# Kernel tuning notes

Hardware: AMD Instinct MI355X
Metric: run time of the kernel (lower is better)

Reference implementation:

```python
import jax, jax.numpy as jnp
import numpy as np
from jax.scipy.special import logsumexp

N, T, K, V = 32, 4096, 128, 50000

def setup_inputs() -> dict:
    key = jax.random.key(0)
    ks = jax.random.split(key, 6)
    return {
        "x": jax.random.randint(ks[0], (N, T), 0, V, dtype=jnp.int64),
        "start_w": jax.random.normal(ks[1], (K, 1), dtype=jnp.float32),
        "start_b": jax.random.normal(ks[2], (K,), dtype=jnp.float32),
        "cluster_trans_w": jax.random.uniform(ks[3], (K * K, 1), dtype=jnp.float32, minval=-1.0, maxval=1.0),
        "emb_cluster_w": jax.random.normal(ks[4], (K, K), dtype=jnp.float32),
        "cluster_vocab_w": jax.random.uniform(ks[5], (V, K), dtype=jnp.float32, minval=-1.0, maxval=1.0),
    }

def reference(x, start_w, start_b, cluster_trans_w, emb_cluster_w, cluster_vocab_w):
    # dummy = ones(N,1) => Linear(1,.) collapses to weight[:,0] (+ bias), identical per batch row
    tran = jax.nn.log_softmax(cluster_trans_w[:, 0].reshape(K, K), axis=-1)      # (K,K) log p(k'|k)
    alpha0 = jnp.broadcast_to(start_w[:, 0] + start_b, (N, K))                    # (N,K)
    # Emissions[k,v] = log_softmax_v(emb_cluster.weight[k] @ cluster_vocab.weight.T)
    emis_t = jax.nn.log_softmax(emb_cluster_w @ cluster_vocab_w.T, axis=-1).T     # (V,K)

    def step(alpha, w_t):
        a = logsumexp(alpha[:, :, None] + tran[None, :, :], axis=1)               # (N,K)
        a = a + emis_t[w_t]                                                        # gather emission log-probs
        return a, None

    alpha_T, _ = jax.lax.scan(step, alpha0, x.T)                                  # scan over T timesteps
    return -jnp.mean(logsumexp(alpha_T, axis=1))
```

## Files before the change

kernel.cpp:

```cpp
#include <hip/hip_runtime.h>

typedef unsigned int uint;
typedef unsigned short ushort;
typedef uint4 uint4_a __attribute__((may_alias));
typedef uint ui4v __attribute__((ext_vector_type(4)));
typedef float fx4 __attribute__((ext_vector_type(4)));
typedef short s8v __attribute__((ext_vector_type(8)));

__device__ __forceinline__ uint bfpack(float a, float b) {
  uint ua = __float_as_uint(a), ub = __float_as_uint(b);
  ua += 0x7fffu + ((ua >> 16) & 1u);
  ub += 0x7fffu + ((ub >> 16) & 1u);
  return (ua >> 16) | (ub & 0xffff0000u);
}
__device__ __forceinline__ float bflo(uint d) { return __uint_as_float(d << 16); }
__device__ __forceinline__ float bfhi(uint d) { return __uint_as_float(d & 0xffff0000u); }
__device__ __forceinline__ ushort bfr(float s) {
  return (ushort)((__float_as_uint(s) + 0x8000u) >> 16);
}

#if __has_builtin(__builtin_amdgcn_fdot2_f32_bf16)
#define HAVE_BFDOT 1
typedef __bf16 v2bf __attribute__((ext_vector_type(2)));
__device__ __forceinline__ float dot2bf(uint a, uint b, float c) {
  return __builtin_amdgcn_fdot2_f32_bf16(__builtin_bit_cast(v2bf, a),
                                         __builtin_bit_cast(v2bf, b), c, false);
}
#else
#define HAVE_BFDOT 0
#endif

__global__ void k_tran(const float* __restrict__ w, uint* __restrict__ Tcol) {
  __shared__ float rowLSE[128];
  int tid = threadIdx.x;
  const float4* w4 = (const float4*)(w + tid * 128);
  float se = 0.f;
  #pragma unroll 8
  for (int i = 0; i < 32; ++i) {
    float4 v = w4[i];
    se += __expf(v.x) + __expf(v.y) + __expf(v.z) + __expf(v.w);
  }
  rowLSE[tid] = __logf(se);
  __syncthreads();
  int c = tid;
  for (int j = 0; j < 64; ++j) {
    float a = __expf(w[(2 * j) * 128 + c]     - rowLSE[2 * j]);
    float b = __expf(w[(2 * j + 1) * 128 + c] - rowLSE[2 * j + 1]);
    Tcol[c * 64 + j] = bfpack(a, b);
  }
}

__global__ __launch_bounds__(256) void k_logits(const float* __restrict__ emb,
    const float* __restrict__ vocab, uint* __restrict__ qtbl,
    float* __restrict__ S_glob, int V) {
  __shared__ float S_part[128];
  int tid = threadIdx.x;
  int kt = tid & 15, vt = tid >> 4;
  int k0 = kt * 8;
  int vbase = blockIdx.x * 64 + vt * 4;
  if (tid < 128) S_part[tid] = 0.f;
  __syncthreads();

  float acc[4][8];
  #pragma unroll
  for (int i = 0; i < 4; ++i)
    #pragma unroll
    for (int r = 0; r < 8; ++r) acc[i][r] = 0.f;

  int vidx[4];
  #pragma unroll
  for (int i = 0; i < 4; ++i) { int vv = vbase + i; vidx[i] = (vv < V) ? vv : (V - 1); }

  const float4* emb4 = (const float4*)emb;
  const float4* voc4 = (const float4*)vocab;
  for (int jb = 0; jb < 32; ++jb) {
    float4 e4[8];
    #pragma unroll
    for (int r = 0; r < 8; ++r) e4[r] = emb4[(k0 + r) * 32 + jb];
    #pragma unroll
    for (int i = 0; i < 4; ++i) {
      float4 va = voc4[(size_t)vidx[i] * 32 + jb];
      #pragma unroll
      for (int r = 0; r < 8; ++r)
        acc[i][r] += va.x * e4[r].x + va.y * e4[r].y + va.z * e4[r].z + va.w * e4[r].w;
    }
  }

  float sume[8];
  #pragma unroll
  for (int r = 0; r < 8; ++r) sume[r] = 0.f;
  #pragma unroll
  for (int i = 0; i < 4; ++i) {
    int vv = vbase + i;
    if (vv < V) {
      #pragma unroll
      for (int r = 0; r < 8; ++r) sume[r] += __expf(acc[i][r]);
      uint4 st;
      st.x = bfpack(acc[i][0], acc[i][1]);
      st.y = bfpack(acc[i][2], acc[i][3]);
      st.z = bfpack(acc[i][4], acc[i][5]);
      st.w = bfpack(acc[i][6], acc[i][7]);
      *((uint4*)(qtbl + (size_t)vv * 64) + kt) = st;
    }
  }
  #pragma unroll
  for (int r = 0; r < 8; ++r) atomicAdd(&S_part[k0 + r], sume[r]);
  __syncthreads();
  if (tid < 128) atomicAdd(&S_glob[tid], S_part[tid]);
}

__global__ __launch_bounds__(256) void k_qtab(uint* __restrict__ qtbl,
    const float* __restrict__ S_glob, float* __restrict__ Emax, int V) {
  int tid = threadIdx.x;
  int l = tid & 63;
  int v = blockIdx.x * 4 + (tid >> 6);
  if (v >= V) return;
  float2 S2 = ((const float2*)S_glob)[l];
  float z0 = __logf(S2.x), z1 = __logf(S2.y);
  size_t off = (size_t)v * 64 + l;
  uint d = qtbl[off];
  float e0 = bflo(d) - z0, e1 = bfhi(d) - z1;
  float m = fmaxf(e0, e1);
  #pragma unroll
  for (int s = 1; s < 64; s <<= 1) m = fmaxf(m, __shfl_xor(m, s, 64));
  float q0 = __expf(e0 - m), q1 = __expf(e1 - m);
  qtbl[off] = bfpack(q0, q1);
  if (l == 0) Emax[v] = m;
}

#define REPB(M) M(0,0) M(0,1) M(0,2) M(0,3) M(1,0) M(1,1) M(1,2) M(1,3) \
                M(2,0) M(2,1) M(2,2) M(2,3) M(3,0) M(3,1) M(3,2) M(3,3) \
                M(4,0) M(4,1) M(4,2) M(4,3) M(5,0) M(5,1) M(5,2) M(5,3) \
                M(6,0) M(6,1) M(6,2) M(6,3) M(7,0) M(7,1) M(7,2) M(7,3)

#define MFMA(a, b, c) __builtin_amdgcn_mfma_f32_16x16x32_bf16( \
    __builtin_bit_cast(s8v, a), __builtin_bit_cast(s8v, b), c, 0, 0, 0)

#define NTCHAIN(nt, BIN) \
  fx4 cc##nt = MFMA(tb##nt##_0, BIN##0, zz4); \
  cc##nt = MFMA(tb##nt##_1, BIN##1, cc##nt); \
  cc##nt = MFMA(tb##nt##_2, BIN##2, cc##nt); \
  cc##nt = MFMA(tb##nt##_3, BIN##3, cc##nt);

#define PKPAIR(CCA, CCB, QA, QB, DOUT) { \
  float f0 = bflo(QA.x) * rs, f1 = bfhi(QA.x) * rs; \
  float f2 = bflo(QA.y) * rs, f3 = bfhi(QA.y) * rs; \
  float s0 = CCA.x * f0, s1 = CCA.y * f1, s2 = CCA.z * f2, s3 = CCA.w * f3; \
  fm = fmaxf(fm, fmaxf(fmaxf(s0, s1), fmaxf(s2, s3))); \
  uint p0, p1, p2, p3; \
  asm("v_cvt_pk_bf16_f32 %0, %1, %2" : "=v"(p0) : "v"(s0), "v"(s1)); \
  asm("v_cvt_pk_bf16_f32 %0, %1, %2" : "=v"(p1) : "v"(s2), "v"(s3)); \
  float g0 = bflo(QB.x) * rs, g1 = bfhi(QB.x) * rs; \
  float g2 = bflo(QB.y) * rs, g3 = bfhi(QB.y) * rs; \
  float t0 = CCB.x * g0, t1 = CCB.y * g1, t2 = CCB.z * g2, t3 = CCB.w * g3; \
  fm = fmaxf(fm, fmaxf(fmaxf(t0, t1), fmaxf(t2, t3))); \
  asm("v_cvt_pk_bf16_f32 %0, %1, %2" : "=v"(p2) : "v"(t0), "v"(t1)); \
  asm("v_cvt_pk_bf16_f32 %0, %1, %2" : "=v"(p3) : "v"(t2), "v"(t3)); \
  DOUT.x = p0; DOUT.y = p1; DOUT.z = p2; DOUT.w = p3; }

#define PKPAIR_NR(CCA, CCB, QA, QB, DOUT) { \
  float s0 = CCA.x * bflo(QA.x), s1 = CCA.y * bfhi(QA.x); \
  float s2 = CCA.z * bflo(QA.y), s3 = CCA.w * bfhi(QA.y); \
  uint p0, p1, p2, p3; \
  asm("v_cvt_pk_bf16_f32 %0, %1, %2" : "=v"(p0) : "v"(s0), "v"(s1)); \
  asm("v_cvt_pk_bf16_f32 %0, %1, %2" : "=v"(p1) : "v"(s2), "v"(s3)); \
  float t0 = CCB.x * bflo(QB.x), t1 = CCB.y * bfhi(QB.x); \
  float t2 = CCB.z * bflo(QB.y), t3 = CCB.w * bfhi(QB.y); \
  asm("v_cvt_pk_bf16_f32 %0, %1, %2" : "=v"(p2) : "v"(t0), "v"(t1)); \
  asm("v_cvt_pk_bf16_f32 %0, %1, %2" : "=v"(p3) : "v"(t2), "v"(t3)); \
  DOUT.x = p0; DOUT.y = p1; DOUT.z = p2; DOUT.w = p3; }

#define QLD(dst, tk, i) dst = *(const uint2*)(qtbl + ((size_t)(tk) << 6) + 8 * (i) + 2 * quad);

#define QRELOAD(Q, TKREG, FBASE) \
  QLD(Q##0, TKREG, 0) QLD(Q##1, TKREG, 1) QLD(Q##2, TKREG, 2) QLD(Q##3, TKREG, 3) \
  QLD(Q##4, TKREG, 4) QLD(Q##5, TKREG, 5) QLD(Q##6, TKREG, 6) QLD(Q##7, TKREG, 7) \
  { int fi_ = (FBASE) + 4; if (fi_ > 511) fi_ = 511; TKREG = xseg[fi_]; }

#define FOLD_RS(BIN, BOUT, Q, TKREG, FBASE) { \
  rs = 1.0f / fmA;  llacc += __log2f(fmA); \
  NTCHAIN(0, BIN) NTCHAIN(1, BIN) NTCHAIN(2, BIN) NTCHAIN(3, BIN) \
  NTCHAIN(4, BIN) NTCHAIN(5, BIN) NTCHAIN(6, BIN) NTCHAIN(7, BIN) \
  float fm = 0.f; \
  PKPAIR(cc0, cc1, Q##0, Q##1, BOUT##0) \
  PKPAIR(cc2, cc3, Q##2, Q##3, BOUT##1) \
  PKPAIR(cc4, cc5, Q##4, Q##5, BOUT##2) \
  PKPAIR(cc6, cc7, Q##6, Q##7, BOUT##3) \
  QRELOAD(Q, TKREG, FBASE) \
  fm = fmaxf(fm, __shfl_xor(fm, 16, 64)); \
  fm = fmaxf(fm, __shfl_xor(fm, 32, 64)); \
  fmA = fmaxf(fm, 1e-33f); \
}

#define FOLD_NR(BIN, BOUT, Q, TKREG, FBASE) { \
  NTCHAIN(0, BIN) NTCHAIN(1, BIN) NTCHAIN(2, BIN) NTCHAIN(3, BIN) \
  NTCHAIN(4, BIN) NTCHAIN(5, BIN) NTCHAIN(6, BIN) NTCHAIN(7, BIN) \
  PKPAIR_NR(cc0, cc1, Q##0, Q##1, BOUT##0) \
  PKPAIR_NR(cc2, cc3, Q##2, Q##3, BOUT##1) \
  PKPAIR_NR(cc4, cc5, Q##4, Q##5, BOUT##2) \
  PKPAIR_NR(cc6, cc7, Q##6, Q##7, BOUT##3) \
  QRELOAD(Q, TKREG, FBASE) \
}

__global__ __attribute__((amdgpu_flat_work_group_size(512, 512), amdgpu_waves_per_eu(2)))
void k_seg(const int* __restrict__ x, const uint* __restrict__ Tcol,
           const uint* __restrict__ qtbl, uint* __restrict__ Pst,
           float* __restrict__ LLseg) {
  int tid = threadIdx.x;
  int wv = tid >> 6, l = tid & 63, c = l & 15, quad = l >> 4;
  int blk = blockIdx.x;
  const int* xseg = x + (size_t)(blk >> 3) * 4096 + (size_t)(blk & 7) * 512;

  #define DECLB(nt, ks) ui4v tb##nt##_##ks;
  REPB(DECLB)
  {
    #define LOADB(nt, ks) { \
      const uint2* t2_ = (const uint2*)(Tcol + (size_t)(16 * (nt) + c) * 64 + 16 * (ks) + 2 * quad); \
      uint2 lo_ = t2_[0], hi_ = t2_[4]; \
      tb##nt##_##ks.x = lo_.x; tb##nt##_##ks.y = lo_.y; \
      tb##nt##_##ks.z = hi_.x; tb##nt##_##ks.w = hi_.y; }
    REPB(LOADB)
    #define PINB(nt, ks) asm volatile("" : "+a"(tb##nt##_##ks));
    REPB(PINB)
  }

  ui4v Ba0, Ba1, Ba2, Ba3, Bb0, Bb1, Bb2, Bb3;
  {
    uint iv = (quad == (c >> 2)) ? (0x3F80u << (16 * (c & 1))) : 0u;
    int dsel = ((c >> 1) & 1) + 2 * (wv & 1);
    int kssel = wv >> 1;
    Ba0.x = (kssel == 0 && dsel == 0) ? iv : 0u;
    Ba0.y = (kssel == 0 && dsel == 1) ? iv : 0u;
    Ba0.z = (kssel == 0 && dsel == 2) ? iv : 0u;
    Ba0.w = (kssel == 0 && dsel == 3) ? iv : 0u;
    Ba1.x = (kssel == 1 && dsel == 0) ? iv : 0u;
    Ba1.y = (kssel == 1 && dsel == 1) ? iv : 0u;
    Ba1.z = (kssel == 1 && dsel == 2) ? iv : 0u;
    Ba1.w = (kssel == 1 && dsel == 3) ? iv : 0u;
    Ba2.x = (kssel == 2 && dsel == 0) ? iv : 0u;
    Ba2.y = (kssel == 2 && dsel == 1) ? iv : 0u;
    Ba2.z = (kssel == 2 && dsel == 2) ? iv : 0u;
    Ba2.w = (kssel == 2 && dsel == 3) ? iv : 0u;
    Ba3.x = (kssel == 3 && dsel == 0) ? iv : 0u;
    Ba3.y = (kssel == 3 && dsel == 1) ? iv : 0u;
    Ba3.z = (kssel == 3 && dsel == 2) ? iv : 0u;
    Ba3.w = (kssel == 3 && dsel == 3) ? iv : 0u;
    Bb0.x = 0u; Bb0.y = 0u; Bb0.z = 0u; Bb0.w = 0u;
    Bb1 = Bb0; Bb2 = Bb0; Bb3 = Bb0;
  }

  float rs = 1.0f, llacc = 0.0f, fmA = 1.0f;
  fx4 zz4; zz4.x = 0.f; zz4.y = 0.f; zz4.z = 0.f; zz4.w = 0.f;

  int tk0 = xseg[0], tk1 = xseg[1];
  int tkA = xseg[2], tkB = xseg[3];
  uint2 qc0, qc1, qc2, qc3, qc4, qc5, qc6, qc7;
  uint2 qn0, qn1, qn2, qn3, qn4, qn5, qn6, qn7;
  QLD(qc0, tk0, 0) QLD(qc1, tk0, 1) QLD(qc2, tk0, 2) QLD(qc3, tk0, 3)
  QLD(qc4, tk0, 4) QLD(qc5, tk0, 5) QLD(qc6, tk0, 6) QLD(qc7, tk0, 7)
  QLD(qn0, tk1, 0) QLD(qn1, tk1, 1) QLD(qn2, tk1, 2) QLD(qn3, tk1, 3)
  QLD(qn4, tk1, 4) QLD(qn5, tk1, 5) QLD(qn6, tk1, 6) QLD(qn7, tk1, 7)

  if (wv & 1) __builtin_amdgcn_s_sleep(8);

  for (int f4 = 0; f4 < 128; ++f4) {
    int f = f4 * 4;
    FOLD_RS(Ba, Bb, qc, tkA, f)
    FOLD_NR(Bb, Ba, qn, tkB, f + 1)
    FOLD_NR(Ba, Bb, qc, tkA, f + 2)
    FOLD_NR(Bb, Ba, qn, tkB, f + 3)
  }

  size_t pb = (size_t)blk * 8192 + (size_t)(16 * wv + c) * 64;
  uint2 st;
  st.x = Ba0.x; st.y = Ba0.y; *(uint2*)(Pst + pb +  0 + 2 * quad) = st;
  st.x = Ba0.z; st.y = Ba0.w; *(uint2*)(Pst + pb +  8 + 2 * quad) = st;
  st.x = Ba1.x; st.y = Ba1.y; *(uint2*)(Pst + pb + 16 + 2 * quad) = st;
  st.x = Ba1.z; st.y = Ba1.w; *(uint2*)(Pst + pb + 24 + 2 * quad) = st;
  st.x = Ba2.x; st.y = Ba2.y; *(uint2*)(Pst + pb + 32 + 2 * quad) = st;
  st.x = Ba2.z; st.y = Ba2.w; *(uint2*)(Pst + pb + 40 + 2 * quad) = st;
  st.x = Ba3.x; st.y = Ba3.y; *(uint2*)(Pst + pb + 48 + 2 * quad) = st;
  st.x = Ba3.z; st.y = Ba3.w; *(uint2*)(Pst + pb + 56 + 2 * quad) = st;
  if (quad == 0)
    LLseg[(size_t)blk * 128 + 16 * wv + c] = llacc * 0.6931471805599453f;
}

__global__ __launch_bounds__(64, 1) void k_comb(
    const float* __restrict__ start_w, const float* __restrict__ start_b,
    const uint* __restrict__ Pst, const float* __restrict__ LLseg,
    float* __restrict__ chainLL) {
  __shared__ uint al[64] __attribute__((aligned(16)));
  int n = blockIdx.x, l = threadIdx.x;
  float a0i = start_w[2 * l] + start_b[2 * l];
  float a1i = start_w[2 * l + 1] + start_b[2 * l + 1];
  float m = fmaxf(a0i, a1i);
  #pragma unroll
  for (int s = 1; s < 64; s <<= 1) m = fmaxf(m, __shfl_xor(m, s, 64));
  float p0 = __expf(a0i - m), p1 = __expf(a1i - m);
  float tot = p0 + p1;
  #pragma unroll
  for (int s = 1; s < 64; s <<= 1) tot += __shfl_xor(tot, s, 64);
  float LLacc = m + __logf(tot);
  float inv = 1.0f / tot;
  p0 *= inv; p1 *= inv;
  const uint4_a* u4 = (const uint4_a*)al;

  for (int s = 0; s < 8; ++s) {
    float La = LLseg[(size_t)(n * 8 + s) * 128 + 2 * l];
    float Lb = LLseg[(size_t)(n * 8 + s) * 128 + 2 * l + 1];
    float g = fmaxf(La, Lb);
    #pragma unroll
    for (int sh = 1; sh < 64; sh <<= 1) g = fmaxf(g, __shfl_xor(g, sh, 64));
    al[l] = bfpack(p0 * __expf(La - g), p1 * __expf(Lb - g));

    const uint* pb = Pst + (size_t)(n * 8 + s) * 8192;
    float o0 = 0.f, o1 = 0.f;
    #pragma unroll
    for (int i = 0; i < 16; ++i) {
      uint4 uu = u4[i];
      #pragma unroll
      for (int d = 0; d < 4; ++d) {
        uint ad = (d == 0) ? uu.x : (d == 1) ? uu.y : (d == 2) ? uu.z : uu.w;
        uint P0 = pb[(8 * i + 2 * d) * 64 + l];
        uint P1 = pb[(8 * i + 2 * d + 1) * 64 + l];
        float alo = bflo(ad), ahi = bfhi(ad);
        o0 = fmaf(alo, bflo(P0), o0); o0 = fmaf(ahi, bflo(P1), o0);
        o1 = fmaf(alo, bfhi(P0), o1); o1 = fmaf(ahi, bfhi(P1), o1);
      }
    }
    float tt = o0 + o1;
    #pragma unroll
    for (int sh = 1; sh < 64; sh <<= 1) tt += __shfl_xor(tt, sh, 64);
    LLacc += g + __logf(tt);
    float it = 1.0f / tt;
    p0 = o0 * it; p1 = o1 * it;
  }
  if (l == 0) chainLL[n] = LLacc;
}

#define RLU(i) ((uint)__builtin_amdgcn_readlane((int)ud, rbase + (i)))
#if HAVE_BFDOT
#define DOTS \
  uint u0=RLU(0),u1=RLU(1),u2=RLU(2),u3=RLU(3),u4=RLU(4),u5=RLU(5),u6=RLU(6),u7=RLU(7), \
       u8=RLU(8),u9=RLU(9),u10=RLU(10),u11=RLU(11),u12=RLU(12),u13=RLU(13),u14=RLU(14),u15=RLU(15); \
  float A0 = dot2bf(u0, tA0.x, 0.f), A1 = dot2bf(u1, tA0.y, 0.f); \
  float A2 = dot2bf(u2, tA0.z, 0.f), A3 = dot2bf(u3, tA0.w, 0.f); \
  float B0 = dot2bf(u0, tB0.x, 0.f), B1 = dot2bf(u1, tB0.y, 0.f); \
  float B2 = dot2bf(u2, tB0.z, 0.f), B3 = dot2bf(u3, tB0.w, 0.f); \
  A0 = dot2bf(u4, tA1.x, A0); A1 = dot2bf(u5, tA1.y, A1); \
  A2 = dot2bf(u6, tA1.z, A2); A3 = dot2bf(u7, tA1.w, A3); \
  B0 = dot2bf(u4, tB1.x, B0); B1 = dot2bf(u5, tB1.y, B1); \
  B2 = dot2bf(u6, tB1.z, B2); B3 = dot2bf(u7, tB1.w, B3); \
  A0 = dot2bf(u8, tA2.x, A0); A1 = dot2bf(u9, tA2.y, A1); \
  A2 = dot2bf(u10, tA2.z, A2); A3 = dot2bf(u11, tA2.w, A3); \
  B0 = dot2bf(u8, tB2.x, B0); B1 = dot2bf(u9, tB2.y, B1); \
  B2 = dot2bf(u10, tB2.z, B2); B3 = dot2bf(u11, tB2.w, B3); \
  A0 = dot2bf(u12, tA3.x, A0); A1 = dot2bf(u13, tA3.y, A1); \
  A2 = dot2bf(u14, tA3.z, A2); A3 = dot2bf(u15, tA3.w, A3); \
  B0 = dot2bf(u12, tB3.x, B0); B1 = dot2bf(u13, tB3.y, B1); \
  B2 = dot2bf(u14, tB3.z, B2); B3 = dot2bf(u15, tB3.w, B3); \
  float Asum = (A0 + A1) + (A2 + A3), Bsum = (B0 + B1) + (B2 + B3);
#else
#define ACC2(i, AA, BB) { uint tu = RLU(i); float lo = bflo(tu), hi = bfhi(tu); \
  AA += lo * fa##i.x; AA += hi * fa##i.y; BB += lo * fb##i.x; BB += hi * fb##i.y; }
#define DOTS \
  float A0 = 0.f, A1 = 0.f, A2 = 0.f, A3 = 0.f; \
  float B0 = 0.f, B1 = 0.f, B2 = 0.f, B3 = 0.f; \
  ACC2(0, A0, B0) ACC2(1, A1, B1) ACC2(2, A2, B2) ACC2(3, A3, B3) \
  ACC2(4, A0, B0) ACC2(5, A1, B1) ACC2(6, A2, B2) ACC2(7, A3, B3) \
  ACC2(8, A0, B0) ACC2(9, A1, B1) ACC2(10, A2, B2) ACC2(11, A3, B3) \
  ACC2(12, A0, B0) ACC2(13, A1, B1) ACC2(14, A2, B2) ACC2(15, A3, B3) \
  float Asum = (A0 + A1) + (A2 + A3), Bsum = (B0 + B1) + (B2 + B3);
#endif

#define STEPF(j, p) { \
  DOTS \
  *(float2*)&partLDS[(p) * 640 + l * 10 + 2 * wv] = make_float2(Asum, Bsum); \
  asm volatile("s_waitcnt lgkmcnt(0)\ns_barrier" ::: "memory"); \
  const float2* pr = (const float2*)&partLDS[(p) * 640 + l * 10]; \
  float2 x0 = pr[0], x1 = pr[1], x2 = pr[2], x3 = pr[3]; \
  float s0 = (x0.x + x1.x) + (x2.x + x3.x); \
  float s1 = (x0.y + x1.y) + (x2.y + x3.y); \
  float nu0 = s0 * bflo(qc##j), nu1 = s1 * bfhi(qc##j); \
  qc##j = qtbl[(size_t)tk##j * 64 + l]; \
  tk##j = xrow[(tbase + (j) + 16) & 4095]; \
  if ((j) == 7) { \
    float tt = nu0 + nu1; \
    for (int s = 1; s < 64; s <<= 1) tt += __shfl_xor(tt, s, 64); \
    LLacc += __logf(tt); \
    float it = 1.0f / tt; nu0 *= it; nu1 *= it; \
  } \
  ud = bfpack(nu0, nu1); }

__global__ __launch_bounds__(256, 1) void k_chain(const int* __restrict__ x,
    const float* __restrict__ start_w, const float* __restrict__ start_b,
    const uint* __restrict__ Tcol, const uint* __restrict__ qtbl,
    float* __restrict__ chainLL) {
  __shared__ float partLDS[1280];
  int n = blockIdx.x;
  int l = threadIdx.x & 63;
  int wv = __builtin_amdgcn_readfirstlane((int)(threadIdx.x >> 6));
  int rbase = wv * 16;
  const int* xrow = x + (size_t)n * 4096;

  const uint4* ca = (const uint4*)(Tcol + (2 * l) * 64 + rbase);
  const uint4* cb = (const uint4*)(Tcol + (2 * l + 1) * 64 + rbase);
  uint4 tA0 = ca[0], tA1 = ca[1], tA2 = ca[2], tA3 = ca[3];
  uint4 tB0 = cb[0], tB1 = cb[1], tB2 = cb[2], tB3 = cb[3];
#if !HAVE_BFDOT
  float2 fa0 = make_float2(bflo(tA0.x), bfhi(tA0.x)), fa1 = make_float2(bflo(tA0.y), bfhi(tA0.y));
  float2 fa2 = make_float2(bflo(tA0.z), bfhi(tA0.z)), fa3 = make_float2(bflo(tA0.w), bfhi(tA0.w));
  float2 fa4 = make_float2(bflo(tA1.x), bfhi(tA1.x)), fa5 = make_float2(bflo(tA1.y), bfhi(tA1.y));
  float2 fa6 = make_float2(bflo(tA1.z), bfhi(tA1.z)), fa7 = make_float2(bflo(tA1.w), bfhi(tA1.w));
  float2 fa8 = make_float2(bflo(tA2.x), bfhi(tA2.x)), fa9 = make_float2(bflo(tA2.y), bfhi(tA2.y));
  float2 fa10 = make_float2(bflo(tA2.z), bfhi(tA2.z)), fa11 = make_float2(bflo(tA2.w), bfhi(tA2.w));
  float2 fa12 = make_float2(bflo(tA3.x), bfhi(tA3.x)), fa13 = make_float2(bflo(tA3.y), bfhi(tA3.y));
  float2 fa14 = make_float2(bflo(tA3.z), bfhi(tA3.z)), fa15 = make_float2(bflo(tA3.w), bfhi(tA3.w));
  float2 fb0 = make_float2(bflo(tB0.x), bfhi(tB0.x)), fb1 = make_float2(bflo(tB0.y), bfhi(tB0.y));
  float2 fb2 = make_float2(bflo(tB0.z), bfhi(tB0.z)), fb3 = make_float2(bflo(tB0.w), bfhi(tB0.w));
  float2 fb4 = make_float2(bflo(tB1.x), bfhi(tB1.x)), fb5 = make_float2(bflo(tB1.y), bfhi(tB1.y));
  float2 fb6 = make_float2(bflo(tB1.z), bfhi(tB1.z)), fb7 = make_float2(bflo(tB1.w), bfhi(tB1.w));
  float2 fb8 = make_float2(bflo(tB2.x), bfhi(tB2.x)), fb9 = make_float2(bflo(tB2.y), bfhi(tB2.y));
  float2 fb10 = make_float2(bflo(tB2.z), bfhi(tB2.z)), fb11 = make_float2(bflo(tB2.w), bfhi(tB2.w));
  float2 fb12 = make_float2(bflo(tB3.x), bfhi(tB3.x)), fb13 = make_float2(bflo(tB3.y), bfhi(tB3.y));
  float2 fb14 = make_float2(bflo(tB3.z), bfhi(tB3.z)), fb15 = make_float2(bflo(tB3.w), bfhi(tB3.w));
#endif

  float a0i = start_w[2 * l] + start_b[2 * l];
  float a1i = start_w[2 * l + 1] + start_b[2 * l + 1];
  float m = fmaxf(a0i, a1i);
  #pragma unroll
  for (int s = 1; s < 64; s <<= 1) m = fmaxf(m, __shfl_xor(m, s, 64));
  float p0 = __expf(a0i - m), p1 = __expf(a1i - m);
  float tot = p0 + p1;
  #pragma unroll
  for (int s = 1; s < 64; s <<= 1) tot += __shfl_xor(tot, s, 64);
  float LLacc = m + __logf(tot);
  float inv = 1.0f / tot;
  uint ud = bfpack(p0 * inv, p1 * inv);

  uint qc0 = qtbl[(size_t)xrow[0] * 64 + l], qc1 = qtbl[(size_t)xrow[1] * 64 + l];
  uint qc2 = qtbl[(size_t)xrow[2] * 64 + l], qc3 = qtbl[(size_t)xrow[3] * 64 + l];
  uint qc4 = qtbl[(size_t)xrow[4] * 64 + l], qc5 = qtbl[(size_t)xrow[5] * 64 + l];
  uint qc6 = qtbl[(size_t)xrow[6] * 64 + l], qc7 = qtbl[(size_t)xrow[7] * 64 + l];
  int tk0 = xrow[8],  tk1 = xrow[9],  tk2 = xrow[10], tk3 = xrow[11];
  int tk4 = xrow[12], tk5 = xrow[13], tk6 = xrow[14], tk7 = xrow[15];

  for (int t8 = 0; t8 < 512; ++t8) {
    int tbase = t8 * 8;
    STEPF(0, 0) STEPF(1, 1) STEPF(2, 0) STEPF(3, 1)
    STEPF(4, 0) STEPF(5, 1) STEPF(6, 0) STEPF(7, 1)
  }
  if (l == 0 && wv == 0) chainLL[n] = LLacc;
}

__global__ __launch_bounds__(256) void k_emaxsum(const int* __restrict__ x,
    const float* __restrict__ Emax, float* __restrict__ sumE, int NT) {
  int idx = blockIdx.x * 256 + threadIdx.x;
  float s = 0.f;
  for (; idx < NT; idx += 128 * 256) s += Emax[x[idx]];
  #pragma unroll
  for (int mk = 1; mk < 64; mk <<= 1) s += __shfl_xor(s, mk, 64);
  if ((threadIdx.x & 63) == 0) atomicAdd(sumE, s);
}

__global__ void k_final(const float* __restrict__ chainLL, const float* __restrict__ sumE,
                        float* __restrict__ out, int N) {
  int l = threadIdx.x;
  float v = (l < N) ? chainLL[l] : 0.f;
  #pragma unroll
  for (int mk = 1; mk < 64; mk <<= 1) v += __shfl_xor(v, mk, 64);
  if (l == 0) out[0] = -(v + sumE[0]) / (float)N;
}

extern "C" void kernel_launch(void* const* d_in, const int* in_sizes, int n_in,
                              void* d_out, int out_size, void* d_ws, size_t ws_size,
                              hipStream_t stream) {
  if (n_in < 6) return;
  const int*   x       = (const int*)d_in[0];
  const float* start_w = (const float*)d_in[1];
  const float* start_b = (const float*)d_in[2];
  const float* trans_w = (const float*)d_in[3];
  const float* emb_w   = (const float*)d_in[4];
  const float* vocab_w = (const float*)d_in[5];
  int NT = in_sizes[0];
  int N  = NT / 4096;
  int V  = in_sizes[5] / 128;

  char* ws = (char*)d_ws;
  float* S_glob  = (float*)(ws + 0);
  float* sumE    = (float*)(ws + 512);
  float* chainLL = (float*)(ws + 768);
  uint*  Tcol    = (uint*)(ws + 1024);
  float* Emax    = (float*)(ws + 36864);
  uint*  qtbl    = (uint*)(ws + 262144);
  size_t pst_off = 262144 + (size_t)V * 256;
  uint*  Pst     = (uint*)(ws + pst_off);
  size_t llseg_off = pst_off + (size_t)N * 8 * 8192 * 4;
  float* LLseg   = (float*)(ws + llseg_off);
  size_t need    = llseg_off + (size_t)N * 8 * 128 * 4 + 64;

  hipMemsetAsync(d_ws, 0, 1024, stream);
  k_tran<<<dim3(1), dim3(128), 0, stream>>>(trans_w, Tcol);
  k_logits<<<dim3((V + 63) / 64), dim3(256), 0, stream>>>(emb_w, vocab_w, qtbl, S_glob, V);
  k_qtab<<<dim3((V + 3) / 4), dim3(256), 0, stream>>>(qtbl, S_glob, Emax, V);
  if (ws_size >= need) {
    k_seg<<<dim3(N * 8), dim3(512), 0, stream>>>(x, Tcol, qtbl, Pst, LLseg);
    k_comb<<<dim3(N), dim3(64), 0, stream>>>(start_w, start_b, Pst, LLseg, chainLL);
  } else {
    k_chain<<<dim3(N), dim3(256), 0, stream>>>(x, start_w, start_b, Tcol, qtbl, chainLL);
  }
  k_emaxsum<<<dim3(128), dim3(256), 0, stream>>>(x, Emax, sumE, NT);
  k_final<<<dim3(1), dim3(64), 0, stream>>>(chainLL, sumE, (float*)d_out, N);
}
```

Measured before the change: 717.6 us.

## Interleave bf16 packing with k-slice-ordered MFMA accumulation across recurrence steps

Reorders the per-step matrix product so that each packed 32-wide slice of the state feeds eight independent MFMA accumulators (one per output tile) as soon as it is packed. This replaces eight tiles that each ran a 4-deep dependent MFMA chain after all packing had finished. The aim is to overlap VALU packing and scaling with MFMA execution and to hide MFMA dependency latency in the serial recurrence. In exchange it keeps two sets of 8 fp32 accumulator vectors live, which raises register pressure, and it computes one extra unused product at loop end.

```diff
diff --git a/kernel.cpp b/kernel.cpp
--- a/kernel.cpp
+++ b/kernel.cpp
@@ -136,11 +136,16 @@
 #define MFMA(a, b, c) __builtin_amdgcn_mfma_f32_16x16x32_bf16( \
     __builtin_bit_cast(s8v, a), __builtin_bit_cast(s8v, b), c, 0, 0, 0)
 
-#define NTCHAIN(nt, BIN) \
-  fx4 cc##nt = MFMA(tb##nt##_0, BIN##0, zz4); \
-  cc##nt = MFMA(tb##nt##_1, BIN##1, cc##nt); \
-  cc##nt = MFMA(tb##nt##_2, BIN##2, cc##nt); \
-  cc##nt = MFMA(tb##nt##_3, BIN##3, cc##nt);
+#define MST0(OUT, BN) \
+  OUT##0 = MFMA(tb0_0, BN, zz4); OUT##1 = MFMA(tb1_0, BN, zz4); \
+  OUT##2 = MFMA(tb2_0, BN, zz4); OUT##3 = MFMA(tb3_0, BN, zz4); \
+  OUT##4 = MFMA(tb4_0, BN, zz4); OUT##5 = MFMA(tb5_0, BN, zz4); \
+  OUT##6 = MFMA(tb6_0, BN, zz4); OUT##7 = MFMA(tb7_0, BN, zz4);
+#define MSTA(OUT, BN, ks) \
+  OUT##0 = MFMA(tb0_##ks, BN, OUT##0); OUT##1 = MFMA(tb1_##ks, BN, OUT##1); \
+  OUT##2 = MFMA(tb2_##ks, BN, OUT##2); OUT##3 = MFMA(tb3_##ks, BN, OUT##3); \
+  OUT##4 = MFMA(tb4_##ks, BN, OUT##4); OUT##5 = MFMA(tb5_##ks, BN, OUT##5); \
+  OUT##6 = MFMA(tb6_##ks, BN, OUT##6); OUT##7 = MFMA(tb7_##ks, BN, OUT##7);
 
 #define PKPAIR(CCA, CCB, QA, QB, DOUT) { \
   float f0 = bflo(QA.x) * rs, f1 = bfhi(QA.x) * rs; \
@@ -177,28 +182,32 @@
   QLD(Q##4, TKREG, 4) QLD(Q##5, TKREG, 5) QLD(Q##6, TKREG, 6) QLD(Q##7, TKREG, 7) \
   { int fi_ = (FBASE) + 4; if (fi_ > 511) fi_ = 511; TKREG = xseg[fi_]; }
 
-#define FOLD_RS(BIN, BOUT, Q, TKREG, FBASE) { \
+#define SLOT_RS(CIN, COUT, Q, TKREG, FBASE) { \
   rs = 1.0f / fmA;  llacc += __log2f(fmA); \
-  NTCHAIN(0, BIN) NTCHAIN(1, BIN) NTCHAIN(2, BIN) NTCHAIN(3, BIN) \
-  NTCHAIN(4, BIN) NTCHAIN(5, BIN) NTCHAIN(6, BIN) NTCHAIN(7, BIN) \
   float fm = 0.f; \
-  PKPAIR(cc0, cc1, Q##0, Q##1, BOUT##0) \
-  PKPAIR(cc2, cc3, Q##2, Q##3, BOUT##1) \
-  PKPAIR(cc4, cc5, Q##4, Q##5, BOUT##2) \
-  PKPAIR(cc6, cc7, Q##6, Q##7, BOUT##3) \
+  PKPAIR(CIN##0, CIN##1, Q##0, Q##1, Bs0) \
+  MST0(COUT, Bs0) \
+  PKPAIR(CIN##2, CIN##3, Q##2, Q##3, Bs1) \
+  MSTA(COUT, Bs1, 1) \
+  PKPAIR(CIN##4, CIN##5, Q##4, Q##5, Bs2) \
+  MSTA(COUT, Bs2, 2) \
+  PKPAIR(CIN##6, CIN##7, Q##6, Q##7, Bs3) \
+  MSTA(COUT, Bs3, 3) \
   QRELOAD(Q, TKREG, FBASE) \
   fm = fmaxf(fm, __shfl_xor(fm, 16, 64)); \
   fm = fmaxf(fm, __shfl_xor(fm, 32, 64)); \
   fmA = fmaxf(fm, 1e-33f); \
 }
 
-#define FOLD_NR(BIN, BOUT, Q, TKREG, FBASE) { \
-  NTCHAIN(0, BIN) NTCHAIN(1, BIN) NTCHAIN(2, BIN) NTCHAIN(3, BIN) \
-  NTCHAIN(4, BIN) NTCHAIN(5, BIN) NTCHAIN(6, BIN) NTCHAIN(7, BIN) \
-  PKPAIR_NR(cc0, cc1, Q##0, Q##1, BOUT##0) \
-  PKPAIR_NR(cc2, cc3, Q##2, Q##3, BOUT##1) \
-  PKPAIR_NR(cc4, cc5, Q##4, Q##5, BOUT##2) \
-  PKPAIR_NR(cc6, cc7, Q##6, Q##7, BOUT##3) \
+#define SLOT_NR(CIN, COUT, Q, TKREG, FBASE) { \
+  PKPAIR_NR(CIN##0, CIN##1, Q##0, Q##1, Bs0) \
+  MST0(COUT, Bs0) \
+  PKPAIR_NR(CIN##2, CIN##3, Q##2, Q##3, Bs1) \
+  MSTA(COUT, Bs1, 1) \
+  PKPAIR_NR(CIN##4, CIN##5, Q##4, Q##5, Bs2) \
+  MSTA(COUT, Bs2, 2) \
+  PKPAIR_NR(CIN##6, CIN##7, Q##6, Q##7, Bs3) \
+  MSTA(COUT, Bs3, 3) \
   QRELOAD(Q, TKREG, FBASE) \
 }
 
@@ -224,33 +233,34 @@
     REPB(PINB)
   }
 
-  ui4v Ba0, Ba1, Ba2, Ba3, Bb0, Bb1, Bb2, Bb3;
+  ui4v Bs0, Bs1, Bs2, Bs3;
   {
     uint iv = (quad == (c >> 2)) ? (0x3F80u << (16 * (c & 1))) : 0u;
     int dsel = ((c >> 1) & 1) + 2 * (wv & 1);
     int kssel = wv >> 1;
-    Ba0.x = (kssel == 0 && dsel == 0) ? iv : 0u;
-    Ba0.y = (kssel == 0 && dsel == 1) ? iv : 0u;
-    Ba0.z = (kssel == 0 && dsel == 2) ? iv : 0u;
-    Ba0.w = (kssel == 0 && dsel == 3) ? iv : 0u;
-    Ba1.x = (kssel == 1 && dsel == 0) ? iv : 0u;
-    Ba1.y = (kssel == 1 && dsel == 1) ? iv : 0u;
-    Ba1.z = (kssel == 1 && dsel == 2) ? iv : 0u;
-    Ba1.w = (kssel == 1 && dsel == 3) ? iv : 0u;
-    Ba2.x = (kssel == 2 && dsel == 0) ? iv : 0u;
-    Ba2.y = (kssel == 2 && dsel == 1) ? iv : 0u;
-    Ba2.z = (kssel == 2 && dsel == 2) ? iv : 0u;
-    Ba2.w = (kssel == 2 && dsel == 3) ? iv : 0u;
-    Ba3.x = (kssel == 3 && dsel == 0) ? iv : 0u;
-    Ba3.y = (kssel == 3 && dsel == 1) ? iv : 0u;
-    Ba3.z = (kssel == 3 && dsel == 2) ? iv : 0u;
-    Ba3.w = (kssel == 3 && dsel == 3) ? iv : 0u;
-    Bb0.x = 0u; Bb0.y = 0u; Bb0.z = 0u; Bb0.w = 0u;
-    Bb1 = Bb0; Bb2 = Bb0; Bb3 = Bb0;
+    Bs0.x = (kssel == 0 && dsel == 0) ? iv : 0u;
+    Bs0.y = (kssel == 0 && dsel == 1) ? iv : 0u;
+    Bs0.z = (kssel == 0 && dsel == 2) ? iv : 0u;
+    Bs0.w = (kssel == 0 && dsel == 3) ? iv : 0u;
+    Bs1.x = (kssel == 1 && dsel == 0) ? iv : 0u;
+    Bs1.y = (kssel == 1 && dsel == 1) ? iv : 0u;
+    Bs1.z = (kssel == 1 && dsel == 2) ? iv : 0u;
+    Bs1.w = (kssel == 1 && dsel == 3) ? iv : 0u;
+    Bs2.x = (kssel == 2 && dsel == 0) ? iv : 0u;
+    Bs2.y = (kssel == 2 && dsel == 1) ? iv : 0u;
+    Bs2.z = (kssel == 2 && dsel == 2) ? iv : 0u;
+    Bs2.w = (kssel == 2 && dsel == 3) ? iv : 0u;
+    Bs3.x = (kssel == 3 && dsel == 0) ? iv : 0u;
+    Bs3.y = (kssel == 3 && dsel == 1) ? iv : 0u;
+    Bs3.z = (kssel == 3 && dsel == 2) ? iv : 0u;
+    Bs3.w = (kssel == 3 && dsel == 3) ? iv : 0u;
   }
 
   float rs = 1.0f, llacc = 0.0f, fmA = 1.0f;
   fx4 zz4; zz4.x = 0.f; zz4.y = 0.f; zz4.z = 0.f; zz4.w = 0.f;
+
+  fx4 cA0, cA1, cA2, cA3, cA4, cA5, cA6, cA7;
+  fx4 cB0, cB1, cB2, cB3, cB4, cB5, cB6, cB7;
 
   int tk0 = xseg[0], tk1 = xseg[1];
   int tkA = xseg[2], tkB = xseg[3];
@@ -261,26 +271,28 @@
   QLD(qn0, tk1, 0) QLD(qn1, tk1, 1) QLD(qn2, tk1, 2) QLD(qn3, tk1, 3)
   QLD(qn4, tk1, 4) QLD(qn5, tk1, 5) QLD(qn6, tk1, 6) QLD(qn7, tk1, 7)
 
+  MST0(cA, Bs0) MSTA(cA, Bs1, 1) MSTA(cA, Bs2, 2) MSTA(cA, Bs3, 3)
+
   if (wv & 1) __builtin_amdgcn_s_sleep(8);
 
   for (int f4 = 0; f4 < 128; ++f4) {
     int f = f4 * 4;
-    FOLD_RS(Ba, Bb, qc, tkA, f)
-    FOLD_NR(Bb, Ba, qn, tkB, f + 1)
-    FOLD_NR(Ba, Bb, qc, tkA, f + 2)
-    FOLD_NR(Bb, Ba, qn, tkB, f + 3)
+    SLOT_RS(cA, cB, qc, tkA, f)
+    SLOT_NR(cB, cA, qn, tkB, f + 1)
+    SLOT_NR(cA, cB, qc, tkA, f + 2)
+    SLOT_NR(cB, cA, qn, tkB, f + 3)
   }
 
   size_t pb = (size_t)blk * 8192 + (size_t)(16 * wv + c) * 64;
   uint2 st;
-  st.x = Ba0.x; st.y = Ba0.y; *(uint2*)(Pst + pb +  0 + 2 * quad) = st;
-  st.x = Ba0.z; st.y = Ba0.w; *(uint2*)(Pst + pb +  8 + 2 * quad) = st;
-  st.x = Ba1.x; st.y = Ba1.y; *(uint2*)(Pst + pb + 16 + 2 * quad) = st;
-  st.x = Ba1.z; st.y = Ba1.w; *(uint2*)(Pst + pb + 24 + 2 * quad) = st;
-  st.x = Ba2.x; st.y = Ba2.y; *(uint2*)(Pst + pb + 32 + 2 * quad) = st;
-  st.x = Ba2.z; st.y = Ba2.w; *(uint2*)(Pst + pb + 40 + 2 * quad) = st;
-  st.x = Ba3.x; st.y = Ba3.y; *(uint2*)(Pst + pb + 48 + 2 * quad) = st;
-  st.x = Ba3.z; st.y = Ba3.w; *(uint2*)(Pst + pb + 56 + 2 * quad) = st;
+  st.x = Bs0.x; st.y = Bs0.y; *(uint2*)(Pst + pb +  0 + 2 * quad) = st;
+  st.x = Bs0.z; st.y = Bs0.w; *(uint2*)(Pst + pb +  8 + 2 * quad) = st;
+  st.x = Bs1.x; st.y = Bs1.y; *(uint2*)(Pst + pb + 16 + 2 * quad) = st;
+  st.x = Bs1.z; st.y = Bs1.w; *(uint2*)(Pst + pb + 24 + 2 * quad) = st;
+  st.x = Bs2.x; st.y = Bs2.y; *(uint2*)(Pst + pb + 32 + 2 * quad) = st;
+  st.x = Bs2.z; st.y = Bs2.w; *(uint2*)(Pst + pb + 40 + 2 * quad) = st;
+  st.x = Bs3.x; st.y = Bs3.y; *(uint2*)(Pst + pb + 48 + 2 * quad) = st;
+  st.x = Bs3.z; st.y = Bs3.w; *(uint2*)(Pst + pb + 56 + 2 * quad) = st;
   if (quad == 0)
     LLseg[(size_t)blk * 128 + 16 * wv + c] = llacc * 0.6931471805599453f;
 }
```

New measurement: 725.7 us. No clear change (+1.1%).
